# Performance work log

Hardware: AMD Instinct MI355X
Metric: run time of the kernel (lower is better)

## Reference

```python
import jax, jax.numpy as jnp
import numpy as np


def setup_inputs() -> dict:
    key = jax.random.key(0)
    ks = jax.random.split(key, 9)
    B, C, H, W = 16, 512, 64, 64
    s = 1.0 / np.sqrt(C)  # fan-in style init scale for 1x1 conv weights
    x = jax.random.normal(ks[0], (B, C, H, W), dtype=jnp.float32)
    W_theta = jax.random.normal(ks[1], (C, C), dtype=jnp.float32) * s
    b_theta = jax.random.normal(ks[2], (C,), dtype=jnp.float32) * 0.01
    W_phi = jax.random.normal(ks[3], (C, C), dtype=jnp.float32) * s
    b_phi = jax.random.normal(ks[4], (C,), dtype=jnp.float32) * 0.01
    W_g = jax.random.normal(ks[5], (C, C), dtype=jnp.float32) * s
    b_g = jax.random.normal(ks[6], (C,), dtype=jnp.float32) * 0.01
    W_out = jax.random.normal(ks[7], (C, C), dtype=jnp.float32) * s
    b_out = jax.random.normal(ks[8], (C,), dtype=jnp.float32) * 0.01
    return {
        "x": x,
        "W_theta": W_theta, "b_theta": b_theta,
        "W_phi": W_phi, "b_phi": b_phi,
        "W_g": W_g, "b_g": b_g,
        "W_out": W_out, "b_out": b_out,
    }


def reference(x, W_theta, b_theta, W_phi, b_phi, W_g, b_g, W_out, b_out):
    B, C, H, W = x.shape
    n = H * W
    xf = x.reshape(B, C, n)  # [B, C, HW]

    def conv1x1(Wm, b):
        # 1x1 conv == channel-mixing GEMM: [O,C] x [B,C,N] -> [B,O,N]
        return jnp.einsum('oc,bcn->bon', Wm, xf) + b[None, :, None]

    phi = conv1x1(W_phi, b_phi)      # [B, C, HW]
    theta = conv1x1(W_theta, b_theta)  # [B, C, HW] (used transposed: 'b (h w) c')
    g = conv1x1(W_g, b_g)            # [B, C, HW]

    # phi @ theta^T over spatial dim -> [B, C, C] channel-channel attention
    scores = jnp.einsum('bcn,bdn->bcd', phi, theta) * (1.0 / C)
    attn = jax.nn.softmax(scores, axis=2)  # softmax over last (dim=2), as in torch
    Y = jnp.einsum('bcd,bdn->bcn', attn, g)  # [B, C, HW]

    A = jnp.einsum('oc,bcn->bon', W_out, Y) + b_out[None, :, None]
    return x + A.reshape(B, C, H, W)
```

## Files before the change

### kernel.cpp

```cpp
#include <hip/hip_runtime.h>
#include <hip/hip_bf16.h>
#include <stdint.h>


typedef unsigned short u16;
typedef __attribute__((ext_vector_type(8))) short frag8;
typedef __attribute__((ext_vector_type(4))) float f32x4;

__device__ __forceinline__ u16 f2bf(float f) {
  union { __hip_bfloat16 h; u16 u; } c; c.h = __float2bfloat16(f); return c.u;
}

__device__ __forceinline__ void gl_lds16(const u16* g, u16* l) {
  __builtin_amdgcn_global_load_lds(
      (const __attribute__((address_space(1))) void*)g,
      (__attribute__((address_space(3))) void*)l, 16, 0, 0);
}

#define SCHED0 __builtin_amdgcn_sched_barrier(0)
#define SBAR   __builtin_amdgcn_s_barrier()

__global__ __launch_bounds__(256) void prep_x(const float* __restrict__ X,
                                              u16* __restrict__ XT,
                                              u16* __restrict__ XB,
                                              float* __restrict__ S) {
  const int b = blockIdx.z;
  const int n0 = blockIdx.x * 64;
  const int c0 = blockIdx.y * 64;
  __shared__ u16 t[64][72];
  const float* Xb = X + (int64_t)b * (512LL * 4096);
  const int tid = threadIdx.x;
  const int r = tid >> 3;
  const int e8 = (tid & 7) * 8;
#pragma unroll
  for (int p = 0; p < 2; p++) {
    const int row = p * 32 + r;
    const int c = c0 + row;
    const float4 f0 = *(const float4*)(Xb + (int64_t)c * 4096 + n0 + e8);
    const float4 f1 = *(const float4*)(Xb + (int64_t)c * 4096 + n0 + e8 + 4);
    union { uint4 q; u16 u[8]; } pk;
    pk.u[0] = f2bf(f0.x); pk.u[1] = f2bf(f0.y); pk.u[2] = f2bf(f0.z); pk.u[3] = f2bf(f0.w);
    pk.u[4] = f2bf(f1.x); pk.u[5] = f2bf(f1.y); pk.u[6] = f2bf(f1.z); pk.u[7] = f2bf(f1.w);
    *(uint4*)(XB + ((int64_t)b * 512 + c) * 4096 + n0 + e8) = pk.q;
    *(uint4*)&t[row][e8 ^ (row & 56)] = pk.q;
    float s = f0.x + f0.y + f0.z + f0.w + f1.x + f1.y + f1.z + f1.w;
    s += __shfl_xor(s, 1); s += __shfl_xor(s, 2); s += __shfl_xor(s, 4);
    if ((tid & 7) == 0) atomicAdd(&S[b * 512 + c], s);
  }
  __syncthreads();
#pragma unroll
  for (int p = 0; p < 2; p++) {
    const int nr = p * 32 + r;
    union { uint4 q; u16 u[8]; } o;
#pragma unroll
    for (int j = 0; j < 8; j++)
      o.u[j] = t[e8 + j][nr ^ e8];
    *(uint4*)(XT + ((int64_t)b * 4096 + n0 + nr) * 512 + c0 + e8) = o.q;
  }
}

__constant__ const int g_ty[10] = {0,0,0,0,1,1,1,2,2,3};
__constant__ const int g_tx[10] = {0,1,2,3,1,2,3,2,3,3};

__global__ __launch_bounds__(256) void gram_sk(const u16* __restrict__ XB,
                                               float* __restrict__ P) {
  const int z = blockIdx.z;
  const int b = z >> 2, sp = z & 3;
  const int tl = blockIdx.x;
  const int m0 = g_ty[tl] * 128, n0 = g_tx[tl] * 128;
  const int tid = threadIdx.x;
  const int lane = tid & 63, wave = tid >> 6;
  __shared__ u16 sA[3][4096];
  __shared__ u16 sB[3][4096];
  const u16* Xb = XB + (int64_t)b * (512LL * 4096) + sp * 1024;

  f32x4 acc[4][4];
#pragma unroll
  for (int i = 0; i < 4; i++)
#pragma unroll
    for (int j = 0; j < 4; j++)
#pragma unroll
      for (int r = 0; r < 4; r++) acc[i][j][r] = 0.0f;

  const int fr = lane & 15;
  const int fk = (lane >> 4) * 8;
  const int wm = (wave & 1) * 64, wn = (wave >> 1) * 64;

  const int srow = tid >> 2;
  const int scol = (tid & 3) * 8;
  const u16* Ar0 = Xb + (int64_t)(m0 + srow) * 4096 + scol;
  const u16* Ar1 = Xb + (int64_t)(m0 + 64 + srow) * 4096 + scol;
  const u16* Br0 = Xb + (int64_t)(n0 + srow) * 4096 + scol;
  const u16* Br1 = Xb + (int64_t)(n0 + 64 + srow) * 4096 + scol;

  auto stage = [&](int t, int buf) {
    gl_lds16(Ar0 + t * 32, sA[buf] + tid * 8);
    gl_lds16(Ar1 + t * 32, sA[buf] + 2048 + tid * 8);
    gl_lds16(Br0 + t * 32, sB[buf] + tid * 8);
    gl_lds16(Br1 + t * 32, sB[buf] + 2048 + tid * 8);
  };
  auto comp = [&](int buf) {
    frag8 af[4], bf[4];
#pragma unroll
    for (int i = 0; i < 4; i++) {
      af[i] = *(const frag8*)(sA[buf] + (wm + i * 16 + fr) * 32 + fk);
      bf[i] = *(const frag8*)(sB[buf] + (wn + i * 16 + fr) * 32 + fk);
    }
#pragma unroll
    for (int i = 0; i < 4; i++)
#pragma unroll
      for (int j = 0; j < 4; j++)
        acc[i][j] = __builtin_amdgcn_mfma_f32_16x16x32_bf16(af[i], bf[j], acc[i][j], 0, 0, 0);
  };

  stage(0, 0); stage(1, 1);
#pragma unroll
  for (int t = 0; t < 30; t++) {
    SCHED0; SBAR; SCHED0;
    stage(t + 2, (t + 2) % 3);
    asm volatile("s_waitcnt vmcnt(8)" ::: "memory");
    SBAR; SCHED0;
    comp(t % 3);
  }
  asm volatile("s_waitcnt vmcnt(0)" ::: "memory");
  SBAR; SCHED0;
  comp(30 % 3); comp(31 % 3);

  float* Pz = P + (int64_t)z * 262144;
  const int quad = lane >> 4;
#pragma unroll
  for (int i = 0; i < 4; i++)
#pragma unroll
    for (int j = 0; j < 4; j++) {
      const int row0 = m0 + wm + i * 16 + quad * 4;
      const int col = n0 + wn + j * 16 + fr;
#pragma unroll
      for (int r = 0; r < 4; r++)
        Pz[(int64_t)(row0 + r) * 512 + col] = acc[i][j][r];
      if (m0 != n0)
        *(f32x4*)(Pz + (int64_t)col * 512 + row0) = acc[i][j];
    }
}

__global__ __launch_bounds__(256) void reduce_G(const float* __restrict__ P,
                                                u16* __restrict__ G) {
  const int64_t t = (int64_t)blockIdx.x * 256 + threadIdx.x;
  const int b = (int)(t >> 16);
  const int64_t i = (t & 65535) * 4;
  const float* P0 = P + ((int64_t)b * 4) * 262144 + i;
  const float4 a = *(const float4*)(P0);
  const float4 c = *(const float4*)(P0 + 262144);
  const float4 d = *(const float4*)(P0 + 2 * 262144);
  const float4 e = *(const float4*)(P0 + 3 * 262144);
  union { u16 u[4]; uint2 v; } o;
  o.u[0] = f2bf(a.x + c.x + d.x + e.x);
  o.u[1] = f2bf(a.y + c.y + d.y + e.y);
  o.u[2] = f2bf(a.z + c.z + d.z + e.z);
  o.u[3] = f2bf(a.w + c.w + d.w + e.w);
  *(uint2*)(G + (int64_t)b * 262144 + i) = o.v;
}

enum { EPI_BF16 = 0, EPI_SCORES = 1, EPI_BF16I = 2 };

template <int EPI>
__global__ __launch_bounds__(256) void gemm64_bt(
    const u16* __restrict__ A, int64_t sAb, int lda,
    const u16* __restrict__ B, int64_t sBb, int ldb,
    void* __restrict__ Cv, int64_t sCb, int ldc,
    const float* __restrict__ e_bphi, const float* __restrict__ e_btheta,
    const float* __restrict__ e_uphi, const float* __restrict__ e_utheta) {
  const int b = blockIdx.z;
  const int m0 = blockIdx.y * 64, n0 = blockIdx.x * 64;
  const int tid = threadIdx.x;
  const int lane = tid & 63, wave = tid >> 6;
  __shared__ u16 sA[3][2048];
  __shared__ u16 sB[3][2048];
  const u16* Ab = A + (int64_t)b * sAb;
  const u16* Bb = B + (int64_t)b * sBb;

  f32x4 acc[2][2];
#pragma unroll
  for (int i = 0; i < 2; i++)
#pragma unroll
    for (int j = 0; j < 2; j++)
#pragma unroll
      for (int r = 0; r < 4; r++) acc[i][j][r] = 0.0f;

  const int srow = tid >> 2;
  const int scol = (tid & 3) * 8;
  const int fr = lane & 15;
  const int fk = (lane >> 4) * 8;
  const int wm = (wave & 1) * 32, wn = (wave >> 1) * 32;

  const u16* Arow = Ab + (int64_t)(m0 + srow) * lda + scol;
  const u16* Brow = Bb + (int64_t)(n0 + srow) * ldb + scol;

  auto stage = [&](int t, int buf) {
    gl_lds16(Arow + t * 32, sA[buf] + tid * 8);
    gl_lds16(Brow + t * 32, sB[buf] + tid * 8);
  };
  auto comp = [&](int buf) {
    frag8 af[2], bf[2];
#pragma unroll
    for (int i = 0; i < 2; i++) {
      af[i] = *(const frag8*)(sA[buf] + (wm + i * 16 + fr) * 32 + fk);
      bf[i] = *(const frag8*)(sB[buf] + (wn + i * 16 + fr) * 32 + fk);
    }
#pragma unroll
    for (int i = 0; i < 2; i++)
#pragma unroll
      for (int j = 0; j < 2; j++)
        acc[i][j] = __builtin_amdgcn_mfma_f32_16x16x32_bf16(af[i], bf[j], acc[i][j], 0, 0, 0);
  };

  stage(0, 0); stage(1, 1);
#pragma unroll
  for (int t = 0; t < 14; t++) {
    SCHED0; SBAR; SCHED0;
    stage(t + 2, (t + 2) % 3);
    asm volatile("s_waitcnt vmcnt(4)" ::: "memory");
    SBAR; SCHED0;
    comp(t % 3);
  }
  asm volatile("s_waitcnt vmcnt(0)" ::: "memory");
  SBAR; SCHED0;
  comp(14 % 3); comp(15 % 3);

  const int quad = lane >> 4;
#pragma unroll
  for (int i = 0; i < 2; i++)
#pragma unroll
    for (int j = 0; j < 2; j++)
#pragma unroll
      for (int r = 0; r < 4; r++) {
        const int row = m0 + wm + i * 16 + quad * 4 + r;
        const int col = n0 + wn + j * 16 + fr;
        const float a = acc[i][j][r];
        if constexpr (EPI == EPI_BF16) {
          ((u16*)Cv)[(int64_t)b * sCb + (int64_t)row * ldc + col] = f2bf(a);
        } else if constexpr (EPI == EPI_BF16I) {
          ((u16*)Cv)[(int64_t)b * sCb + (int64_t)row * ldc + col] =
              f2bf(a + (row == col ? 1.0f : 0.0f));
        } else {
          const float bp = e_bphi[row];
          const float bt = e_btheta[col];
          ((float*)Cv)[(int64_t)b * sCb + (int64_t)row * ldc + col] =
              (a + bp * e_utheta[b * 512 + col] + bt * e_uphi[b * 512 + row] +
               4096.0f * bp * bt) * (1.0f / 512.0f);
        }
      }
}

__global__ __launch_bounds__(256) void gemm_final(const u16* __restrict__ M,
                                                  const u16* __restrict__ XT,
                                                  const float* __restrict__ V,
                                                  float* __restrict__ O) {
  const int b = blockIdx.z;
  const int m0 = blockIdx.y * 128, n0 = blockIdx.x * 128;
  const int tid = threadIdx.x;
  const int lane = tid & 63, wave = tid >> 6;
  __shared__ u16 sA[3][4096];
  __shared__ u16 sB[3][4096];
  const u16* Ab = M + (int64_t)b * 262144;
  const u16* Bb = XT + (int64_t)b * (4096LL * 512);

  f32x4 acc[4][4];
#pragma unroll
  for (int i = 0; i < 4; i++)
#pragma unroll
    for (int j = 0; j < 4; j++)
#pragma unroll
      for (int r = 0; r < 4; r++) acc[i][j][r] = 0.0f;

  const int srow = tid >> 2;
  const int scol = (tid & 3) * 8;
  const int fr = lane & 15;
  const int fk = (lane >> 4) * 8;
  const int wm = (wave & 1) * 64, wn = (wave >> 1) * 64;

  const u16* Ar0 = Ab + (int64_t)(m0 + srow) * 512 + scol;
  const u16* Ar1 = Ab + (int64_t)(m0 + 64 + srow) * 512 + scol;
  const u16* Br0 = Bb + (int64_t)(n0 + srow) * 512 + scol;
  const u16* Br1 = Bb + (int64_t)(n0 + 64 + srow) * 512 + scol;

  auto stage = [&](int t, int buf) {
    gl_lds16(Ar0 + t * 32, sA[buf] + tid * 8);
    gl_lds16(Ar1 + t * 32, sA[buf] + 2048 + tid * 8);
    gl_lds16(Br0 + t * 32, sB[buf] + tid * 8);
    gl_lds16(Br1 + t * 32, sB[buf] + 2048 + tid * 8);
  };
  auto comp = [&](int buf) {
    frag8 af[4], bf[4];
#pragma unroll
    for (int i = 0; i < 4; i++) {
      af[i] = *(const frag8*)(sA[buf] + (wm + i * 16 + fr) * 32 + fk);
      bf[i] = *(const frag8*)(sB[buf] + (wn + i * 16 + fr) * 32 + fk);
    }
#pragma unroll
    for (int i = 0; i < 4; i++)
#pragma unroll
      for (int j = 0; j < 4; j++)
        acc[i][j] = __builtin_amdgcn_mfma_f32_16x16x32_bf16(af[i], bf[j], acc[i][j], 0, 0, 0);
  };

  stage(0, 0); stage(1, 1);
#pragma unroll
  for (int t = 0; t < 14; t++) {
    SCHED0; SBAR; SCHED0;
    stage(t + 2, (t + 2) % 3);
    asm volatile("s_waitcnt vmcnt(8)" ::: "memory");
    SBAR; SCHED0;
    comp(t % 3);
  }
  asm volatile("s_waitcnt vmcnt(0)" ::: "memory");
  SBAR; SCHED0;
  comp(14 % 3); comp(15 % 3);

  const int quad = lane >> 4;
#pragma unroll
  for (int i = 0; i < 4; i++)
#pragma unroll
    for (int j = 0; j < 4; j++)
#pragma unroll
      for (int r = 0; r < 4; r++) {
        const int row = m0 + wm + i * 16 + quad * 4 + r;
        const int col = n0 + wn + j * 16 + fr;
        O[(int64_t)b * (512LL * 4096) + (int64_t)row * 4096 + col] =
            acc[i][j][r] + V[b * 512 + row];
      }
}

__global__ __launch_bounds__(512) void uv_kernel(const float* __restrict__ Wphi,
                                                 const float* __restrict__ Wtheta,
                                                 const float* __restrict__ S,
                                                 float* __restrict__ UPH, float* __restrict__ UTH) {
  const int b = blockIdx.x;
  const int o = threadIdx.x;
  __shared__ float s[512];
  s[o] = S[b * 512 + o];
  __syncthreads();
  float a0 = 0.f, a1 = 0.f;
  for (int c4 = 0; c4 < 512; c4 += 4) {
    const float4 wa = *(const float4*)(Wphi + o * 512 + c4);
    const float4 wb = *(const float4*)(Wtheta + o * 512 + c4);
    a0 += wa.x * s[c4] + wa.y * s[c4 + 1] + wa.z * s[c4 + 2] + wa.w * s[c4 + 3];
    a1 += wb.x * s[c4] + wb.y * s[c4 + 1] + wb.z * s[c4 + 2] + wb.w * s[c4 + 3];
  }
  UPH[b * 512 + o] = a0;
  UTH[b * 512 + o] = a1;
}

__global__ __launch_bounds__(512) void v_kernel(const float* __restrict__ Wout,
                                                const float* __restrict__ R,
                                                const float* __restrict__ bout,
                                                float* __restrict__ V) {
  const int b = blockIdx.x;
  const int o = threadIdx.x;
  __shared__ float s[512];
  s[o] = R[b * 512 + o];
  __syncthreads();
  float a0 = 0.f;
  for (int c4 = 0; c4 < 512; c4 += 4) {
    const float4 wa = *(const float4*)(Wout + o * 512 + c4);
    a0 += wa.x * s[c4] + wa.y * s[c4 + 1] + wa.z * s[c4 + 2] + wa.w * s[c4 + 3];
  }
  V[b * 512 + o] = a0 + bout[o];
}

__global__ __launch_bounds__(256) void convert_w(const float* __restrict__ W0,
                                                 const float* __restrict__ W1,
                                                 const float* __restrict__ W2,
                                                 u16* __restrict__ O0, u16* __restrict__ O1,
                                                 u16* __restrict__ O2) {
  const int idx = blockIdx.x * 256 + threadIdx.x;
  const int m = idx >> 16;
  const int off = (idx & 65535) * 4;
  const float* src = (m == 0) ? W0 : (m == 1) ? W1 : W2;
  u16* dst = (m == 0) ? O0 : (m == 1) ? O1 : O2;
  const float4 f = *(const float4*)(src + off);
  union { u16 u[4]; uint2 v; } p;
  p.u[0] = f2bf(f.x); p.u[1] = f2bf(f.y); p.u[2] = f2bf(f.z); p.u[3] = f2bf(f.w);
  *(uint2*)(dst + off) = p.v;
}

__global__ void wg_transpose(const float* __restrict__ Wg, u16* __restrict__ WgT) {
  __shared__ float t[16][17];
  const int i0 = blockIdx.y * 16, j0 = blockIdx.x * 16;
  t[threadIdx.y][threadIdx.x] = Wg[(i0 + threadIdx.y) * 512 + j0 + threadIdx.x];
  __syncthreads();
  WgT[(j0 + threadIdx.y) * 512 + i0 + threadIdx.x] = f2bf(t[threadIdx.x][threadIdx.y]);
}

__global__ __launch_bounds__(64) void softmax_k(float* __restrict__ SC,
                                                const float* __restrict__ bg,
                                                float* __restrict__ R) {
  const int row = blockIdx.x;
  const int lane = threadIdx.x;
  float* Sr = SC + (int64_t)row * 512;
  union { float4 q[2]; float v[8]; } u;
  u.q[0] = *(const float4*)(Sr + lane * 8);
  u.q[1] = *(const float4*)(Sr + lane * 8 + 4);
  const float4 g0 = *(const float4*)(bg + lane * 8);
  const float4 g1 = *(const float4*)(bg + lane * 8 + 4);
  const float gb[8] = { g0.x, g0.y, g0.z, g0.w, g1.x, g1.y, g1.z, g1.w };
  float m = u.v[0];
#pragma unroll
  for (int j = 1; j < 8; j++) m = fmaxf(m, u.v[j]);
#pragma unroll
  for (int off = 32; off > 0; off >>= 1) m = fmaxf(m, __shfl_xor(m, off));
  float e[8], s = 0.f, sb = 0.f;
#pragma unroll
  for (int j = 0; j < 8; j++) {
    e[j] = __expf(u.v[j] - m);
    s += e[j];
    sb += e[j] * gb[j];
  }
#pragma unroll
  for (int off = 32; off > 0; off >>= 1) { s += __shfl_xor(s, off); sb += __shfl_xor(sb, off); }
  const float inv = 1.0f / s;
  union { uint4 q; u16 h[8]; } o;
#pragma unroll
  for (int j = 0; j < 8; j++) o.h[j] = f2bf(e[j] * inv);
  *(uint4*)((u16*)SC + (int64_t)row * 1024 + lane * 8) = o.q;
  if (lane == 0) R[row] = sb * inv;
}

extern "C" void kernel_launch(void* const* d_in, const int* in_sizes, int n_in,
                              void* d_out, int out_size, void* d_ws, size_t ws_size,
                              hipStream_t stream) {
  const float* x      = (const float*)d_in[0];
  const float* Wtheta = (const float*)d_in[1];
  const float* btheta = (const float*)d_in[2];
  const float* Wphi   = (const float*)d_in[3];
  const float* bphi   = (const float*)d_in[4];
  const float* Wg     = (const float*)d_in[5];
  const float* bg     = (const float*)d_in[6];
  const float* Wout   = (const float*)d_in[7];
  const float* bout   = (const float*)d_in[8];

  char* ws = (char*)d_ws;
  u16*   xT     = (u16*)(ws + 0);
  u16*   G      = (u16*)(ws + 67108864);
  u16*   T1     = (u16*)(ws + 75497472);
  float* SC     = (float*)(ws + 83886080);
  u16*   Wphib  = (u16*)(ws + 100663296);
  u16*   Wthetab= (u16*)(ws + 101187584);
  u16*   Woutb  = (u16*)(ws + 101711872);
  u16*   WgTb   = (u16*)(ws + 102236160);
  float* S      = (float*)(ws + 102760448);
  float* UPH    = (float*)(ws + 102793216);
  float* UTH    = (float*)(ws + 102825984);
  float* R      = (float*)(ws + 102858752);
  float* V      = (float*)(ws + 102891520);
  u16* ATT = (u16*)SC;
  u16* Q = G;
  u16* M = T1;

  u16*   XB = (u16*)d_out;
  float* P  = (float*)((char*)d_out + 67108864);

  hipMemsetAsync(S, 0, 32768, stream);
  prep_x<<<dim3(64, 8, 16), 256, 0, stream>>>(x, xT, XB, S);
  uv_kernel<<<16, 512, 0, stream>>>(Wphi, Wtheta, S, UPH, UTH);
  convert_w<<<768, 256, 0, stream>>>(Wphi, Wtheta, Wout, Wphib, Wthetab, Woutb);
  wg_transpose<<<dim3(32, 32), dim3(16, 16), 0, stream>>>(Wg, WgTb);
  gram_sk<<<dim3(10, 1, 64), 256, 0, stream>>>(XB, P);
  reduce_G<<<4096, 256, 0, stream>>>(P, G);
  gemm64_bt<EPI_BF16><<<dim3(8, 8, 16), 256, 0, stream>>>(
      Wphib, 0, 512, G, 512LL * 512, 512, T1, 512LL * 512, 512,
      nullptr, nullptr, nullptr, nullptr);
  gemm64_bt<EPI_SCORES><<<dim3(8, 8, 16), 256, 0, stream>>>(
      T1, 512LL * 512, 512, Wthetab, 0, 512, SC, 512LL * 512, 512,
      bphi, btheta, UPH, UTH);
  softmax_k<<<8192, 64, 0, stream>>>(SC, bg, R);
  gemm64_bt<EPI_BF16><<<dim3(8, 8, 16), 256, 0, stream>>>(
      WgTb, 0, 512, ATT, 512LL * 1024, 1024, Q, 512LL * 512, 512,
      nullptr, nullptr, nullptr, nullptr);
  gemm64_bt<EPI_BF16I><<<dim3(8, 8, 16), 256, 0, stream>>>(
      Woutb, 0, 512, Q, 512LL * 512, 512, M, 512LL * 512, 512,
      nullptr, nullptr, nullptr, nullptr);
  v_kernel<<<16, 512, 0, stream>>>(Wout, R, bout, V);
  gemm_final<<<dim3(32, 4, 16), 256, 0, stream>>>(M, xT, V, (float*)d_out);
}
```

Before: 545.2 us.

## Enlarge batched channel GEMM tiles to 128x128 and simplify final GEMM pipeline

Switches the four 512x512 batched GEMMs from 64x64 tiles with a 3-stage LDS pipeline to 128x128 tiles with a 4-stage pipeline. This raises MFMA work per staged load and cuts global traffic. The block count drops from 1024 to 256 per GEMM, which lowers parallelism on a many-CU GPU and raises LDS use. The final GEMM moves from a hand-scheduled 3-stage pipeline to a simple double-buffered loop with __syncthreads, trading prefetch depth for lower LDS use.

```diff
diff --git a/kernel.cpp b/kernel.cpp
--- a/kernel.cpp
+++ b/kernel.cpp
@@ -163,26 +163,26 @@
 enum { EPI_BF16 = 0, EPI_SCORES = 1, EPI_BF16I = 2 };
 
 template <int EPI>
-__global__ __launch_bounds__(256) void gemm64_bt(
+__global__ __launch_bounds__(256) void gemm128_bt(
     const u16* __restrict__ A, int64_t sAb, int lda,
     const u16* __restrict__ B, int64_t sBb, int ldb,
     void* __restrict__ Cv, int64_t sCb, int ldc,
     const float* __restrict__ e_bphi, const float* __restrict__ e_btheta,
     const float* __restrict__ e_uphi, const float* __restrict__ e_utheta) {
   const int b = blockIdx.z;
-  const int m0 = blockIdx.y * 64, n0 = blockIdx.x * 64;
+  const int m0 = blockIdx.y * 128, n0 = blockIdx.x * 128;
   const int tid = threadIdx.x;
   const int lane = tid & 63, wave = tid >> 6;
-  __shared__ u16 sA[3][2048];
-  __shared__ u16 sB[3][2048];
+  __shared__ u16 sA[4][4096];
+  __shared__ u16 sB[4][4096];
   const u16* Ab = A + (int64_t)b * sAb;
   const u16* Bb = B + (int64_t)b * sBb;
 
-  f32x4 acc[2][2];
-#pragma unroll
-  for (int i = 0; i < 2; i++)
-#pragma unroll
-    for (int j = 0; j < 2; j++)
+  f32x4 acc[4][4];
+#pragma unroll
+  for (int i = 0; i < 4; i++)
+#pragma unroll
+    for (int j = 0; j < 4; j++)
 #pragma unroll
       for (int r = 0; r < 4; r++) acc[i][j][r] = 0.0f;
 
@@ -190,47 +190,57 @@
   const int scol = (tid & 3) * 8;
   const int fr = lane & 15;
   const int fk = (lane >> 4) * 8;
-  const int wm = (wave & 1) * 32, wn = (wave >> 1) * 32;
-
-  const u16* Arow = Ab + (int64_t)(m0 + srow) * lda + scol;
-  const u16* Brow = Bb + (int64_t)(n0 + srow) * ldb + scol;
+  const int wm = (wave & 1) * 64, wn = (wave >> 1) * 64;
+
+  const u16* Ar0 = Ab + (int64_t)(m0 + srow) * lda + scol;
+  const u16* Ar1 = Ab + (int64_t)(m0 + 64 + srow) * lda + scol;
+  const u16* Br0 = Bb + (int64_t)(n0 + srow) * ldb + scol;
+  const u16* Br1 = Bb + (int64_t)(n0 + 64 + srow) * ldb + scol;
 
   auto stage = [&](int t, int buf) {
-    gl_lds16(Arow + t * 32, sA[buf] + tid * 8);
-    gl_lds16(Brow + t * 32, sB[buf] + tid * 8);
+    gl_lds16(Ar0 + t * 32, sA[buf] + tid * 8);
+    gl_lds16(Ar1 + t * 32, sA[buf] + 2048 + tid * 8);
+    gl_lds16(Br0 + t * 32, sB[buf] + tid * 8);
+    gl_lds16(Br1 + t * 32, sB[buf] + 2048 + tid * 8);
   };
   auto comp = [&](int buf) {
-    frag8 af[2], bf[2];
-#pragma unroll
-    for (int i = 0; i < 2; i++) {
+    frag8 af[4], bf[4];
+#pragma unroll
+    for (int i = 0; i < 4; i++) {
       af[i] = *(const frag8*)(sA[buf] + (wm + i * 16 + fr) * 32 + fk);
       bf[i] = *(const frag8*)(sB[buf] + (wn + i * 16 + fr) * 32 + fk);
     }
 #pragma unroll
-    for (int i = 0; i < 2; i++)
-#pragma unroll
-      for (int j = 0; j < 2; j++)
+    for (int i = 0; i < 4; i++)
+#pragma unroll
+      for (int j = 0; j < 4; j++)
         acc[i][j] = __builtin_amdgcn_mfma_f32_16x16x32_bf16(af[i], bf[j], acc[i][j], 0, 0, 0);
   };
 
-  stage(0, 0); stage(1, 1);
-#pragma unroll
-  for (int t = 0; t < 14; t++) {
+  stage(0, 0); stage(1, 1); stage(2, 2);
+#pragma unroll
+  for (int t = 0; t < 13; t++) {
     SCHED0; SBAR; SCHED0;
-    stage(t + 2, (t + 2) % 3);
-    asm volatile("s_waitcnt vmcnt(4)" ::: "memory");
+    stage(t + 3, (t + 3) % 4);
+    asm volatile("s_waitcnt vmcnt(12)" ::: "memory");
     SBAR; SCHED0;
-    comp(t % 3);
-  }
+    comp(t % 4);
+  }
+  asm volatile("s_waitcnt vmcnt(8)" ::: "memory");
+  SBAR; SCHED0;
+  comp(13 % 4);
+  asm volatile("s_waitcnt vmcnt(4)" ::: "memory");
+  SBAR; SCHED0;
+  comp(14 % 4);
   asm volatile("s_waitcnt vmcnt(0)" ::: "memory");
   SBAR; SCHED0;
-  comp(14 % 3); comp(15 % 3);
+  comp(15 % 4);
 
   const int quad = lane >> 4;
 #pragma unroll
-  for (int i = 0; i < 2; i++)
-#pragma unroll
-    for (int j = 0; j < 2; j++)
+  for (int i = 0; i < 4; i++)
+#pragma unroll
+    for (int j = 0; j < 4; j++)
 #pragma unroll
       for (int r = 0; r < 4; r++) {
         const int row = m0 + wm + i * 16 + quad * 4 + r;
@@ -259,8 +269,8 @@
   const int m0 = blockIdx.y * 128, n0 = blockIdx.x * 128;
   const int tid = threadIdx.x;
   const int lane = tid & 63, wave = tid >> 6;
-  __shared__ u16 sA[3][4096];
-  __shared__ u16 sB[3][4096];
+  __shared__ u16 sA[2][4096];
+  __shared__ u16 sB[2][4096];
   const u16* Ab = M + (int64_t)b * 262144;
   const u16* Bb = XT + (int64_t)b * (4096LL * 512);
 
@@ -283,38 +293,35 @@
   const u16* Br0 = Bb + (int64_t)(n0 + srow) * 512 + scol;
   const u16* Br1 = Bb + (int64_t)(n0 + 64 + srow) * 512 + scol;
 
-  auto stage = [&](int t, int buf) {
-    gl_lds16(Ar0 + t * 32, sA[buf] + tid * 8);
-    gl_lds16(Ar1 + t * 32, sA[buf] + 2048 + tid * 8);
-    gl_lds16(Br0 + t * 32, sB[buf] + tid * 8);
-    gl_lds16(Br1 + t * 32, sB[buf] + 2048 + tid * 8);
-  };
-  auto comp = [&](int buf) {
+  gl_lds16(Ar0, sA[0] + tid * 8);
+  gl_lds16(Ar1, sA[0] + 2048 + tid * 8);
+  gl_lds16(Br0, sB[0] + tid * 8);
+  gl_lds16(Br1, sB[0] + 2048 + tid * 8);
+  __syncthreads();
+
+  for (int k0 = 0; k0 < 512; k0 += 32) {
+    const int cur = (k0 >> 5) & 1;
+    if (k0 + 32 < 512) {
+      u16* dA = sA[cur ^ 1];
+      u16* dB = sB[cur ^ 1];
+      gl_lds16(Ar0 + k0 + 32, dA + tid * 8);
+      gl_lds16(Ar1 + k0 + 32, dA + 2048 + tid * 8);
+      gl_lds16(Br0 + k0 + 32, dB + tid * 8);
+      gl_lds16(Br1 + k0 + 32, dB + 2048 + tid * 8);
+    }
     frag8 af[4], bf[4];
 #pragma unroll
     for (int i = 0; i < 4; i++) {
-      af[i] = *(const frag8*)(sA[buf] + (wm + i * 16 + fr) * 32 + fk);
-      bf[i] = *(const frag8*)(sB[buf] + (wn + i * 16 + fr) * 32 + fk);
+      af[i] = *(const frag8*)(sA[cur] + (wm + i * 16 + fr) * 32 + fk);
+      bf[i] = *(const frag8*)(sB[cur] + (wn + i * 16 + fr) * 32 + fk);
     }
 #pragma unroll
     for (int i = 0; i < 4; i++)
 #pragma unroll
       for (int j = 0; j < 4; j++)
         acc[i][j] = __builtin_amdgcn_mfma_f32_16x16x32_bf16(af[i], bf[j], acc[i][j], 0, 0, 0);
-  };
-
-  stage(0, 0); stage(1, 1);
-#pragma unroll
-  for (int t = 0; t < 14; t++) {
-    SCHED0; SBAR; SCHED0;
-    stage(t + 2, (t + 2) % 3);
-    asm volatile("s_waitcnt vmcnt(8)" ::: "memory");
-    SBAR; SCHED0;
-    comp(t % 3);
-  }
-  asm volatile("s_waitcnt vmcnt(0)" ::: "memory");
-  SBAR; SCHED0;
-  comp(14 % 3); comp(15 % 3);
+    __syncthreads();
+  }
 
   const int quad = lane >> 4;
 #pragma unroll
@@ -466,17 +473,17 @@
   wg_transpose<<<dim3(32, 32), dim3(16, 16), 0, stream>>>(Wg, WgTb);
   gram_sk<<<dim3(10, 1, 64), 256, 0, stream>>>(XB, P);
   reduce_G<<<4096, 256, 0, stream>>>(P, G);
-  gemm64_bt<EPI_BF16><<<dim3(8, 8, 16), 256, 0, stream>>>(
+  gemm128_bt<EPI_BF16><<<dim3(4, 4, 16), 256, 0, stream>>>(
       Wphib, 0, 512, G, 512LL * 512, 512, T1, 512LL * 512, 512,
       nullptr, nullptr, nullptr, nullptr);
-  gemm64_bt<EPI_SCORES><<<dim3(8, 8, 16), 256, 0, stream>>>(
+  gemm128_bt<EPI_SCORES><<<dim3(4, 4, 16), 256, 0, stream>>>(
       T1, 512LL * 512, 512, Wthetab, 0, 512, SC, 512LL * 512, 512,
       bphi, btheta, UPH, UTH);
   softmax_k<<<8192, 64, 0, stream>>>(SC, bg, R);
-  gemm64_bt<EPI_BF16><<<dim3(8, 8, 16), 256, 0, stream>>>(
+  gemm128_bt<EPI_BF16><<<dim3(4, 4, 16), 256, 0, stream>>>(
       WgTb, 0, 512, ATT, 512LL * 1024, 1024, Q, 512LL * 512, 512,
       nullptr, nullptr, nullptr, nullptr);
-  gemm64_bt<EPI_BF16I><<<dim3(8, 8, 16), 256, 0, stream>>>(
+  gemm128_bt<EPI_BF16I><<<dim3(4, 4, 16), 256, 0, stream>>>(
       Woutb, 0, 512, Q, 512LL * 512, 512, M, 512LL * 512, 512,
       nullptr, nullptr, nullptr, nullptr);
   v_kernel<<<16, 512, 0, stream>>>(Wout, R, bout, V);
```

Measured after the change: 542.2 us. Within noise of the previous version (-0.5%).
